# Optimization experiments

Measured on AMD Instinct MI355X. Metric: run time of the kernel, lower is better.

Reference implementation:

```python
import jax, jax.numpy as jnp
import numpy as np

B, S, D = 4, 4096, 1024
P = int(D * 1.333)  # 1364, matches torch int(d_model * proj_factor)
CAP = 15.0
EPS = 1e-6


def _rmsnorm(x, w, eps=EPS):
    xf = x.astype(jnp.float32)
    var = jnp.mean(xf * xf, axis=-1, keepdims=True)
    return w * (xf * jax.lax.rsqrt(var + eps)).astype(x.dtype)


def _softcap_sigmoid(g):
    # sigmoid(cap * tanh(g / cap))
    return jax.nn.sigmoid(CAP * jnp.tanh(g / CAP))


def setup_inputs() -> dict:
    key = jax.random.key(0)
    k0, k1, k2, k3 = jax.random.split(key, 4)
    x = jax.random.normal(k0, (B, S, D), jnp.float32)
    hidden_state = jnp.zeros((B, P), jnp.float32)
    ln_weight = jnp.ones((D,), jnp.float32)
    W_gate = jax.random.normal(k1, (D, 3 * P), jnp.float32) / np.sqrt(D).astype(np.float32)
    W_cell = jax.random.normal(k2, (D, P), jnp.float32) / np.sqrt(D).astype(np.float32)
    W_out = jax.random.normal(k3, (P, D), jnp.float32) / np.sqrt(P).astype(np.float32)
    return {"x": x, "hidden_state": hidden_state, "ln_weight": ln_weight,
            "W_gate": W_gate, "W_cell": W_cell, "W_out": W_out}


def reference(x, hidden_state, ln_weight, W_gate, W_cell, W_out):
    b, s, d = x.shape
    residual = x
    xn = _rmsnorm(x, ln_weight)
    # gate projection -> [b, s, 3, P], unbind gate types
    gates = jnp.einsum('bsd,dk->bsk', xn, W_gate).reshape(b, s, 3, P)
    i_gate = _softcap_sigmoid(gates[:, :, 0])
    f_gate = _softcap_sigmoid(gates[:, :, 1])
    o_gate = _softcap_sigmoid(gates[:, :, 2])
    c_input = jnp.einsum('bsd,dp->bsp', xn, W_cell)

    # sequential linear recurrence: h_t = f_t * h_{t-1} + i_t * tanh(c_t)
    def step(h, inp):
        c_t, i_t, f_t, o_t = inp
        h = f_t * h + i_t * jnp.tanh(c_t)
        return h, o_t * jnp.tanh(h)

    seq = (jnp.swapaxes(c_input, 0, 1), jnp.swapaxes(i_gate, 0, 1),
           jnp.swapaxes(f_gate, 0, 1), jnp.swapaxes(o_gate, 0, 1))  # time-major [s,b,P]
    _, outs = jax.lax.scan(step, hidden_state, seq)
    outputs = jnp.swapaxes(outs, 0, 1)  # [b, s, P]

    out = residual + jnp.einsum('bsp,pd->bsd', outputs, W_out)
    # NOTE: original torch module returns the UNMODIFIED initial hidden_state
    return out, hidden_state
```

## Files before the change

### kernel.cpp

```cpp
#include <hip/hip_runtime.h>
#include <hip/hip_bf16.h>
#include <math.h>
#include <stdint.h>

typedef __bf16 bf16_t;
typedef bf16_t bf16x4 __attribute__((ext_vector_type(4)));
typedef bf16_t bf16x8 __attribute__((ext_vector_type(8)));
typedef float floatx4 __attribute__((ext_vector_type(4)));

#define B_     4
#define S_     4096
#define D_     1024
#define P_     1364
#define P3_    4092
#define NP_    5456
#define NPAD_  5504
#define NB_    5632
#define KPAD_  1408
#define ROWS_  16384
#define CAP_   15.0f
#define EPS_   1e-6f
#define CHUNKS_ 32
#define CLEN_   128

__device__ __forceinline__ float fast_tanh(float x) {
    x = fminf(fmaxf(x, -15.f), 15.f);
    float e = __expf(2.f * x);
    return __fdividef(e - 1.f, e + 1.f);
}
__device__ __forceinline__ float fast_softcap_sig(float g) {
    float t = fast_tanh(g * (1.0f / CAP_));
    return __fdividef(1.f, 1.f + __expf(-CAP_ * t));
}

template <int N>
__device__ __forceinline__ void vmcnt_wait() {
    if constexpr (N == 8)      asm volatile("s_waitcnt vmcnt(8)" ::: "memory");
    else if constexpr (N == 0) asm volatile("s_waitcnt vmcnt(0)" ::: "memory");
}

__global__ __launch_bounds__(256) void rmsnorm_kernel(const float* __restrict__ x,
                                                      const float* __restrict__ w,
                                                      bf16_t* __restrict__ xn) {
    int row = blockIdx.x;
    int tid = threadIdx.x;
    const float4 v = ((const float4*)(x + (size_t)row * D_))[tid];
    float ss = v.x * v.x + v.y * v.y + v.z * v.z + v.w * v.w;
    #pragma unroll
    for (int off = 32; off > 0; off >>= 1) ss += __shfl_down(ss, off);
    __shared__ float red[4];
    if ((tid & 63) == 0) red[tid >> 6] = ss;
    __syncthreads();
    float tot = red[0] + red[1] + red[2] + red[3];
    float scale = rsqrtf(tot * (1.0f / (float)D_) + EPS_);
    const float4 wv = ((const float4*)w)[tid];
    bf16x4 o;
    o[0] = (bf16_t)(v.x * scale * wv.x);
    o[1] = (bf16_t)(v.y * scale * wv.y);
    o[2] = (bf16_t)(v.z * scale * wv.z);
    o[3] = (bf16_t)(v.w * scale * wv.w);
    ((bf16x4*)(xn + (size_t)row * D_))[tid] = o;
}

__global__ __launch_bounds__(256) void pack_wcat(const float* __restrict__ Wg,
                                                 const float* __restrict__ Wc,
                                                 bf16_t* __restrict__ Wt) {
    __shared__ float tile[32][33];
    int kt = blockIdx.x * 32;
    int nt = blockIdx.y * 32;
    int tx = threadIdx.x & 31;
    int ty = threadIdx.x >> 5;
    #pragma unroll
    for (int i = 0; i < 4; i++) {
        int k = kt + ty + 8 * i;
        int n = nt + tx;
        float val = 0.f;
        if (n < P3_)      val = Wg[(size_t)k * P3_ + n];
        else if (n < NP_) val = Wc[(size_t)k * P_ + (n - P3_)];
        tile[ty + 8 * i][tx] = val;
    }
    __syncthreads();
    #pragma unroll
    for (int i = 0; i < 4; i++) {
        int n = nt + ty + 8 * i;
        int k = kt + tx;
        Wt[(size_t)n * D_ + k] = (bf16_t)tile[tx][ty + 8 * i];
    }
}

__global__ __launch_bounds__(256) void pack_wout(const float* __restrict__ Wo,
                                                 bf16_t* __restrict__ Wt) {
    __shared__ float tile[32][33];
    int pt = blockIdx.x * 32;
    int dt = blockIdx.y * 32;
    int tx = threadIdx.x & 31;
    int ty = threadIdx.x >> 5;
    #pragma unroll
    for (int i = 0; i < 4; i++) {
        int p = pt + ty + 8 * i;
        int d = dt + tx;
        float val = (p < P_) ? Wo[(size_t)p * D_ + d] : 0.f;
        tile[ty + 8 * i][tx] = val;
    }
    __syncthreads();
    #pragma unroll
    for (int i = 0; i < 4; i++) {
        int d = dt + ty + 8 * i;
        int p = pt + tx;
        Wt[(size_t)d * KPAD_ + p] = (bf16_t)tile[tx][ty + 8 * i];
    }
}

template <int KTOT, int LDA, int LDB, int LDC, int NX, int EPI>
__global__ __launch_bounds__(512, 2) void gemm8(const bf16_t* __restrict__ A,
                                                const bf16_t* __restrict__ Bt,
                                                const float* __restrict__ res,
                                                void* __restrict__ outv) {
    constexpr int NT = KTOT / 64;
    static_assert(NT >= 4, "NT >= 4");
    __shared__ __align__(16) char smem[131072];

    const int tid  = threadIdx.x;
    const int wid  = tid >> 6;
    const int lane = tid & 63;
    const int l15  = lane & 15;
    const int sl4  = lane >> 4;
    const int sp    = sl4 ^ ((lane >> 1) & 3);
    const int chunk = (lane & 3) ^ ((lane >> 3) & 3);
    const int wrow = (wid >> 2) * 128;
    const int wcol = (wid & 3) * 64;

    constexpr int MCH = (ROWS_ / 256) / 8;
    const int bid = blockIdx.x;
    const int xcd = bid & 7;
    const int idx = bid >> 3;
    const int bx  = idx / MCH;
    const int by  = xcd * MCH + (idx - bx * MCH);
    const int m0 = by * 256, n0 = bx * 256;

    const int srow = wid * 16 + (lane >> 2);
    const bf16_t* Asrc = A  + (size_t)(m0 + srow) * LDA + chunk * 8;
    const bf16_t* Bsrc = Bt + (size_t)(n0 + srow) * LDB + chunk * 8;
    const unsigned ldsA0 = (unsigned)(wid * 1024);
    const unsigned ldsB0 = 32768u + (unsigned)(wid * 1024);

    auto stage = [&](int kt, int buf) {
        #pragma unroll
        for (int kk = 0; kk < 2; kk++) {
            const bf16_t* sa = Asrc + kt * 64 + kk * 32;
            char* da = smem + ((unsigned)buf * 65536u + (unsigned)kk * 16384u + ldsA0);
            __builtin_amdgcn_global_load_lds((const unsigned*)sa, (unsigned*)da, 16, 0, 0);
            __builtin_amdgcn_global_load_lds((const unsigned*)(sa + (size_t)128 * LDA),
                                             (unsigned*)(da + 8192), 16, 0, 0);
            const bf16_t* sb = Bsrc + kt * 64 + kk * 32;
            char* db = smem + ((unsigned)buf * 65536u + (unsigned)kk * 16384u + ldsB0);
            __builtin_amdgcn_global_load_lds((const unsigned*)sb, (unsigned*)db, 16, 0, 0);
            __builtin_amdgcn_global_load_lds((const unsigned*)(sb + (size_t)128 * LDB),
                                             (unsigned*)(db + 8192), 16, 0, 0);
        }
    };
    auto ldA = [&](int buf, int kk, int m) -> bf16x8 {
        return *(const bf16x8*)(smem + (buf * 65536 + kk * 16384 +
                                        (wrow + m * 16 + l15) * 64 + sp * 16));
    };
    auto ldB = [&](int buf, int kk, int n) -> bf16x8 {
        return *(const bf16x8*)(smem + (buf * 65536 + 32768 + kk * 16384 +
                                        (wcol + n * 16 + l15) * 64 + sp * 16));
    };

    floatx4 acc[8][4];
    #pragma unroll
    for (int m = 0; m < 8; m++)
        #pragma unroll
        for (int n = 0; n < 4; n++) acc[m][n] = (floatx4){0.f, 0.f, 0.f, 0.f};

    bf16x8 a0[8], b0v[4], a1[8], b1v[4];

    stage(0, 0);
    stage(1, 1);
    vmcnt_wait<8>();
    __builtin_amdgcn_s_barrier();

    for (int t = 0; t < NT; ++t) {
        const int c = t & 1;
        #pragma unroll
        for (int m = 0; m < 8; m++) a0[m] = ldA(c, 0, m);
        #pragma unroll
        for (int n = 0; n < 4; n++) b0v[n] = ldB(c, 0, n);
        #pragma unroll
        for (int m = 0; m < 8; m++) a1[m] = ldA(c, 1, m);
        #pragma unroll
        for (int n = 0; n < 4; n++) b1v[n] = ldB(c, 1, n);

        __builtin_amdgcn_s_setprio(1);
        #pragma unroll
        for (int m = 0; m < 8; m++)
            #pragma unroll
            for (int n = 0; n < 4; n++)
                acc[m][n] = __builtin_amdgcn_mfma_f32_16x16x32_bf16(a0[m], b0v[n], acc[m][n], 0, 0, 0);
        #pragma unroll
        for (int m = 0; m < 8; m++)
            #pragma unroll
            for (int n = 0; n < 4; n++)
                acc[m][n] = __builtin_amdgcn_mfma_f32_16x16x32_bf16(a1[m], b1v[n], acc[m][n], 0, 0, 0);
        __builtin_amdgcn_s_setprio(0);

        __builtin_amdgcn_s_barrier();
        if (t + 2 < NT) {
            stage(t + 2, c);
            vmcnt_wait<8>();
        } else if (t + 2 == NT) {
            vmcnt_wait<0>();
        }
        __builtin_amdgcn_s_barrier();
    }

    const int crow = m0 + wrow + sl4 * 4;
    const int ccol = n0 + wcol + l15;
    if constexpr (EPI == 0) {
        bf16_t* O = (bf16_t*)outv;
        #pragma unroll
        for (int m = 0; m < 8; m++)
            #pragma unroll
            for (int n = 0; n < 4; n++) {
                const int col = ccol + n * 16;
                if (col < NPAD_) {
                    #pragma unroll
                    for (int r = 0; r < 4; r++) {
                        const int row = crow + m * 16 + r;
                        float g = acc[m][n][r];
                        float v = (col < P3_) ? fast_softcap_sig(g) : fast_tanh(g);
                        O[(size_t)row * LDC + col] = (bf16_t)v;
                    }
                }
            }
    } else {
        float* O = (float*)outv;
        #pragma unroll
        for (int m = 0; m < 8; m++)
            #pragma unroll
            for (int n = 0; n < 4; n++) {
                const int col = ccol + n * 16;
                #pragma unroll
                for (int r = 0; r < 4; r++) {
                    const int row = crow + m * 16 + r;
                    O[(size_t)row * LDC + col] = res[(size_t)row * LDC + col] + acc[m][n][r];
                }
            }
    }
}

__global__ __launch_bounds__(256) void chunk_scan1(const bf16_t* __restrict__ act,
                                                   float* __restrict__ FA) {
    int p = blockIdx.x * 256 + threadIdx.x;
    int c = blockIdx.y;
    int b = blockIdx.z;
    if (p >= P_) return;
    const bf16_t* base = act + (size_t)(b * S_ + c * CLEN_) * NPAD_;
    float F = 1.f, Acc = 0.f;
    for (int t = 0; t < CLEN_; t++) {
        const bf16_t* r = base + (size_t)t * NPAD_;
        float iv = (float)r[p];
        float fv = (float)r[P_ + p];
        float tc = (float)r[P3_ + p];
        Acc = fv * Acc + iv * tc;
        F *= fv;
    }
    size_t idx = (((size_t)b * CHUNKS_ + c) * P_ + p) * 2;
    FA[idx]     = F;
    FA[idx + 1] = Acc;
}

__global__ __launch_bounds__(256) void chunk_scan2(const bf16_t* __restrict__ act,
                                                   const float* __restrict__ FA,
                                                   const float* __restrict__ h0,
                                                   bf16_t* __restrict__ outp) {
    int p = blockIdx.x * 256 + threadIdx.x;
    int c = blockIdx.y;
    int b = blockIdx.z;
    if (p >= KPAD_) return;
    if (p >= P_) {
        bf16_t z = (bf16_t)0.f;
        for (int t = 0; t < CLEN_; t++)
            outp[(size_t)(b * S_ + c * CLEN_ + t) * KPAD_ + p] = z;
        return;
    }
    float h = h0[(size_t)b * P_ + p];
    for (int j = 0; j < c; j++) {
        size_t idx = (((size_t)b * CHUNKS_ + j) * P_ + p) * 2;
        h = FA[idx + 1] + FA[idx] * h;
    }
    const bf16_t* base = act + (size_t)(b * S_ + c * CLEN_) * NPAD_;
    bf16_t* ob = outp + (size_t)(b * S_ + c * CLEN_) * KPAD_;
    for (int t = 0; t < CLEN_; t++) {
        const bf16_t* r = base + (size_t)t * NPAD_;
        float iv = (float)r[p];
        float fv = (float)r[P_ + p];
        float ov = (float)r[2 * P_ + p];
        float tc = (float)r[P3_ + p];
        h = fv * h + iv * tc;
        ob[(size_t)t * KPAD_ + p] = (bf16_t)(ov * fast_tanh(h));
    }
}

__global__ void copy_hidden(const float* __restrict__ hs, float* __restrict__ dst) {
    int i = blockIdx.x * 256 + threadIdx.x;
    if (i < B_ * P_) dst[i] = hs[i];
}

extern "C" void kernel_launch(void* const* d_in, const int* in_sizes, int n_in,
                              void* d_out, int out_size, void* d_ws, size_t ws_size,
                              hipStream_t stream) {
    const float* x   = (const float*)d_in[0];
    const float* hs  = (const float*)d_in[1];
    const float* lnw = (const float*)d_in[2];
    const float* Wg  = (const float*)d_in[3];
    const float* Wc  = (const float*)d_in[4];
    const float* Wo  = (const float*)d_in[5];
    float* out = (float*)d_out;

    char* ws = (char*)d_ws;
    size_t off = 0;
    auto alloc = [&](size_t bytes) {
        void* p = ws + off;
        off += (bytes + 255) & ~(size_t)255;
        return p;
    };
    bf16_t* xn_outp = (bf16_t*)alloc((size_t)ROWS_ * KPAD_ * 2);
    bf16_t* act     = (bf16_t*)alloc((size_t)ROWS_ * NPAD_ * 2);
    bf16_t* WcatT   = (bf16_t*)alloc((size_t)NB_ * D_ * 2);
    bf16_t* WoutT   = (bf16_t*)alloc((size_t)D_ * KPAD_ * 2);
    float*  FA      = (float*)alloc((size_t)B_ * CHUNKS_ * P_ * 2 * 4);

    bf16_t* xn   = xn_outp;
    bf16_t* outp = xn_outp;

    hipLaunchKernelGGL(rmsnorm_kernel, dim3(ROWS_), dim3(256), 0, stream, x, lnw, xn);
    hipLaunchKernelGGL(pack_wcat, dim3(32, NB_ / 32), dim3(256), 0, stream, Wg, Wc, WcatT);
    hipLaunchKernelGGL(pack_wout, dim3(KPAD_ / 32, D_ / 32), dim3(256), 0, stream, Wo, WoutT);

    hipLaunchKernelGGL((gemm8<D_, D_, D_, NPAD_, NB_ / 256, 0>),
                       dim3((NB_ / 256) * (ROWS_ / 256)), dim3(512), 0, stream,
                       xn, WcatT, (const float*)nullptr, (void*)act);

    hipLaunchKernelGGL(chunk_scan1, dim3(6, CHUNKS_, B_), dim3(256), 0, stream, act, FA);
    hipLaunchKernelGGL(chunk_scan2, dim3(6, CHUNKS_, B_), dim3(256), 0, stream, act, FA, hs, outp);

    hipLaunchKernelGGL((gemm8<KPAD_, KPAD_, KPAD_, D_, D_ / 256, 1>),
                       dim3((D_ / 256) * (ROWS_ / 256)), dim3(512), 0, stream,
                       outp, WoutT, x, d_out);

    hipLaunchKernelGGL(copy_hidden, dim3((B_ * P_ + 255) / 256), dim3(256), 0, stream,
                       hs, out + (size_t)ROWS_ * D_);
}
```

Measured before the change: 501.6 us.

## Restructure GEMM main loop into four quadrant phases with interleaved prefetch

Replaces the two-stage-ahead prefetch and monolithic per-tile MFMA block with a one-stage-ahead double buffer. Each k-tile is split into four quadrant sub-phases that interleave LDS fragment reads, A/B global-to-LDS staging and MFMA bursts, with barriers and setprio around each. The aim is to cut register pressure from holding all fragments at once and to spread memory traffic across the compute. In exchange it adds many more barriers per iteration and only one tile of prefetch lead, which may expose global load latency.

```diff
diff --git a/kernel.cpp b/kernel.cpp
--- a/kernel.cpp
+++ b/kernel.cpp
@@ -33,10 +33,8 @@
     return __fdividef(1.f, 1.f + __expf(-CAP_ * t));
 }
 
-template <int N>
-__device__ __forceinline__ void vmcnt_wait() {
-    if constexpr (N == 8)      asm volatile("s_waitcnt vmcnt(8)" ::: "memory");
-    else if constexpr (N == 0) asm volatile("s_waitcnt vmcnt(0)" ::: "memory");
+__device__ __forceinline__ void vmcnt0() {
+    asm volatile("s_waitcnt vmcnt(0)" ::: "memory");
 }
 
 __global__ __launch_bounds__(256) void rmsnorm_kernel(const float* __restrict__ x,
@@ -117,7 +115,7 @@
                                                 const float* __restrict__ res,
                                                 void* __restrict__ outv) {
     constexpr int NT = KTOT / 64;
-    static_assert(NT >= 4, "NT >= 4");
+    static_assert(NT >= 2, "NT >= 2");
     __shared__ __align__(16) char smem[131072];
 
     const int tid  = threadIdx.x;
@@ -144,7 +142,7 @@
     const unsigned ldsA0 = (unsigned)(wid * 1024);
     const unsigned ldsB0 = 32768u + (unsigned)(wid * 1024);
 
-    auto stage = [&](int kt, int buf) {
+    auto stageA = [&](int kt, int buf) {
         #pragma unroll
         for (int kk = 0; kk < 2; kk++) {
             const bf16_t* sa = Asrc + kt * 64 + kk * 32;
@@ -152,6 +150,11 @@
             __builtin_amdgcn_global_load_lds((const unsigned*)sa, (unsigned*)da, 16, 0, 0);
             __builtin_amdgcn_global_load_lds((const unsigned*)(sa + (size_t)128 * LDA),
                                              (unsigned*)(da + 8192), 16, 0, 0);
+        }
+    };
+    auto stageB = [&](int kt, int buf) {
+        #pragma unroll
+        for (int kk = 0; kk < 2; kk++) {
             const bf16_t* sb = Bsrc + kt * 64 + kk * 32;
             char* db = smem + ((unsigned)buf * 65536u + (unsigned)kk * 16384u + ldsB0);
             __builtin_amdgcn_global_load_lds((const unsigned*)sb, (unsigned*)db, 16, 0, 0);
@@ -174,44 +177,82 @@
         #pragma unroll
         for (int n = 0; n < 4; n++) acc[m][n] = (floatx4){0.f, 0.f, 0.f, 0.f};
 
-    bf16x8 a0[8], b0v[4], a1[8], b1v[4];
-
-    stage(0, 0);
-    stage(1, 1);
-    vmcnt_wait<8>();
+    bf16x8 aq[8];
+    bf16x8 bq[4];
+    bf16x8 bq2[4];
+
+    stageA(0, 0);
+    stageB(0, 0);
+    vmcnt0();
     __builtin_amdgcn_s_barrier();
 
     for (int t = 0; t < NT; ++t) {
         const int c = t & 1;
-        #pragma unroll
-        for (int m = 0; m < 8; m++) a0[m] = ldA(c, 0, m);
-        #pragma unroll
-        for (int n = 0; n < 4; n++) b0v[n] = ldB(c, 0, n);
-        #pragma unroll
-        for (int m = 0; m < 8; m++) a1[m] = ldA(c, 1, m);
-        #pragma unroll
-        for (int n = 0; n < 4; n++) b1v[n] = ldB(c, 1, n);
-
+        const bool st = (t + 1 < NT);
+
+        #pragma unroll
+        for (int m = 0; m < 4; m++) { aq[m] = ldA(c, 0, m); aq[m + 4] = ldA(c, 1, m); }
+        #pragma unroll
+        for (int n = 0; n < 2; n++) { bq[n] = ldB(c, 0, n); bq[n + 2] = ldB(c, 1, n); }
+        if (st) stageA(t + 1, c ^ 1);
+        __builtin_amdgcn_s_barrier();
+        asm volatile("s_waitcnt lgkmcnt(0)" ::: "memory");
         __builtin_amdgcn_s_setprio(1);
         #pragma unroll
-        for (int m = 0; m < 8; m++)
-            #pragma unroll
-            for (int n = 0; n < 4; n++)
-                acc[m][n] = __builtin_amdgcn_mfma_f32_16x16x32_bf16(a0[m], b0v[n], acc[m][n], 0, 0, 0);
-        #pragma unroll
-        for (int m = 0; m < 8; m++)
-            #pragma unroll
-            for (int n = 0; n < 4; n++)
-                acc[m][n] = __builtin_amdgcn_mfma_f32_16x16x32_bf16(a1[m], b1v[n], acc[m][n], 0, 0, 0);
+        for (int m = 0; m < 4; m++)
+            #pragma unroll
+            for (int n = 0; n < 2; n++) {
+                acc[m][n] = __builtin_amdgcn_mfma_f32_16x16x32_bf16(aq[m], bq[n], acc[m][n], 0, 0, 0);
+                acc[m][n] = __builtin_amdgcn_mfma_f32_16x16x32_bf16(aq[m + 4], bq[n + 2], acc[m][n], 0, 0, 0);
+            }
         __builtin_amdgcn_s_setprio(0);
-
-        __builtin_amdgcn_s_barrier();
-        if (t + 2 < NT) {
-            stage(t + 2, c);
-            vmcnt_wait<8>();
-        } else if (t + 2 == NT) {
-            vmcnt_wait<0>();
-        }
+        __builtin_amdgcn_s_barrier();
+
+        #pragma unroll
+        for (int n = 0; n < 2; n++) { bq2[n] = ldB(c, 0, n + 2); bq2[n + 2] = ldB(c, 1, n + 2); }
+        if (st) stageB(t + 1, c ^ 1);
+        __builtin_amdgcn_s_barrier();
+        asm volatile("s_waitcnt lgkmcnt(0)" ::: "memory");
+        __builtin_amdgcn_s_setprio(1);
+        #pragma unroll
+        for (int m = 0; m < 4; m++)
+            #pragma unroll
+            for (int n = 0; n < 2; n++) {
+                acc[m][n + 2] = __builtin_amdgcn_mfma_f32_16x16x32_bf16(aq[m], bq2[n], acc[m][n + 2], 0, 0, 0);
+                acc[m][n + 2] = __builtin_amdgcn_mfma_f32_16x16x32_bf16(aq[m + 4], bq2[n + 2], acc[m][n + 2], 0, 0, 0);
+            }
+        __builtin_amdgcn_s_setprio(0);
+        __builtin_amdgcn_s_barrier();
+
+        #pragma unroll
+        for (int m = 0; m < 4; m++) { aq[m] = ldA(c, 0, m + 4); aq[m + 4] = ldA(c, 1, m + 4); }
+        __builtin_amdgcn_s_barrier();
+        asm volatile("s_waitcnt lgkmcnt(0)" ::: "memory");
+        __builtin_amdgcn_s_setprio(1);
+        #pragma unroll
+        for (int m = 0; m < 4; m++)
+            #pragma unroll
+            for (int n = 0; n < 2; n++) {
+                acc[m + 4][n + 2] = __builtin_amdgcn_mfma_f32_16x16x32_bf16(aq[m], bq2[n], acc[m + 4][n + 2], 0, 0, 0);
+                acc[m + 4][n + 2] = __builtin_amdgcn_mfma_f32_16x16x32_bf16(aq[m + 4], bq2[n + 2], acc[m + 4][n + 2], 0, 0, 0);
+            }
+        __builtin_amdgcn_s_setprio(0);
+        __builtin_amdgcn_s_barrier();
+
+        #pragma unroll
+        for (int n = 0; n < 2; n++) { bq[n] = ldB(c, 0, n); bq[n + 2] = ldB(c, 1, n); }
+        __builtin_amdgcn_s_barrier();
+        asm volatile("s_waitcnt lgkmcnt(0)" ::: "memory");
+        __builtin_amdgcn_s_setprio(1);
+        #pragma unroll
+        for (int m = 0; m < 4; m++)
+            #pragma unroll
+            for (int n = 0; n < 2; n++) {
+                acc[m + 4][n] = __builtin_amdgcn_mfma_f32_16x16x32_bf16(aq[m], bq[n], acc[m + 4][n], 0, 0, 0);
+                acc[m + 4][n] = __builtin_amdgcn_mfma_f32_16x16x32_bf16(aq[m + 4], bq[n + 2], acc[m + 4][n], 0, 0, 0);
+            }
+        __builtin_amdgcn_s_setprio(0);
+        vmcnt0();
         __builtin_amdgcn_s_barrier();
     }
 
```

New measurement: 463.5 us. 1.08x faster.

## Replace 256x256 double-buffered GEMM with simpler single-buffered 128x128 tile GEMM

Applied to the files above, without the earlier changes.

Both GEMMs move from a 512-thread kernel with 256x256 output tiles, two LDS stages and hand-placed vmcnt waits to a 256-thread kernel with 128x128 tiles and one LDS stage guarded by __syncthreads. The smaller tile and LDS footprint give more blocks and higher occupancy, and the grid has more blocks to spread across CUs. In exchange it loses load/compute overlap inside a block, halves data reuse per tile (more global and LDS traffic per FLOP), and adds two full barriers per k-step. The result is likely a less efficient GEMM.

```diff
diff --git a/kernel.cpp b/kernel.cpp
--- a/kernel.cpp
+++ b/kernel.cpp
@@ -33,12 +33,6 @@
     return __fdividef(1.f, 1.f + __expf(-CAP_ * t));
 }
 
-template <int N>
-__device__ __forceinline__ void vmcnt_wait() {
-    if constexpr (N == 8)      asm volatile("s_waitcnt vmcnt(8)" ::: "memory");
-    else if constexpr (N == 0) asm volatile("s_waitcnt vmcnt(0)" ::: "memory");
-}
-
 __global__ __launch_bounds__(256) void rmsnorm_kernel(const float* __restrict__ x,
                                                       const float* __restrict__ w,
                                                       bf16_t* __restrict__ xn) {
@@ -111,14 +105,13 @@
     }
 }
 
-template <int KTOT, int LDA, int LDB, int LDC, int NX, int EPI>
-__global__ __launch_bounds__(512, 2) void gemm8(const bf16_t* __restrict__ A,
-                                                const bf16_t* __restrict__ Bt,
-                                                const float* __restrict__ res,
-                                                void* __restrict__ outv) {
+template <int KTOT, int LDA, int LDB, int LDC, int EPI>
+__global__ __launch_bounds__(256) void gemm128(const bf16_t* __restrict__ A,
+                                               const bf16_t* __restrict__ Bt,
+                                               const float* __restrict__ res,
+                                               void* __restrict__ outv) {
     constexpr int NT = KTOT / 64;
-    static_assert(NT >= 4, "NT >= 4");
-    __shared__ __align__(16) char smem[131072];
+    __shared__ __align__(16) char smem[32768];
 
     const int tid  = threadIdx.x;
     const int wid  = tid >> 6;
@@ -127,92 +120,66 @@
     const int sl4  = lane >> 4;
     const int sp    = sl4 ^ ((lane >> 1) & 3);
     const int chunk = (lane & 3) ^ ((lane >> 3) & 3);
-    const int wrow = (wid >> 2) * 128;
-    const int wcol = (wid & 3) * 64;
-
-    constexpr int MCH = (ROWS_ / 256) / 8;
+    const int wrow = (wid >> 1) * 64;
+    const int wcol = (wid & 1) * 64;
+
     const int bid = blockIdx.x;
     const int xcd = bid & 7;
     const int idx = bid >> 3;
-    const int bx  = idx / MCH;
-    const int by  = xcd * MCH + (idx - bx * MCH);
-    const int m0 = by * 256, n0 = bx * 256;
+    const int bx  = idx >> 4;
+    const int by  = xcd * 16 + (idx & 15);
+    const int m0 = by * 128, n0 = bx * 128;
 
     const int srow = wid * 16 + (lane >> 2);
     const bf16_t* Asrc = A  + (size_t)(m0 + srow) * LDA + chunk * 8;
     const bf16_t* Bsrc = Bt + (size_t)(n0 + srow) * LDB + chunk * 8;
-    const unsigned ldsA0 = (unsigned)(wid * 1024);
-    const unsigned ldsB0 = 32768u + (unsigned)(wid * 1024);
-
-    auto stage = [&](int kt, int buf) {
+    const unsigned ldsW = (unsigned)(wid * 1024);
+
+    auto stage = [&](int kt) {
         #pragma unroll
         for (int kk = 0; kk < 2; kk++) {
             const bf16_t* sa = Asrc + kt * 64 + kk * 32;
-            char* da = smem + ((unsigned)buf * 65536u + (unsigned)kk * 16384u + ldsA0);
+            char* da = smem + (unsigned)kk * 8192u + ldsW;
             __builtin_amdgcn_global_load_lds((const unsigned*)sa, (unsigned*)da, 16, 0, 0);
-            __builtin_amdgcn_global_load_lds((const unsigned*)(sa + (size_t)128 * LDA),
-                                             (unsigned*)(da + 8192), 16, 0, 0);
+            __builtin_amdgcn_global_load_lds((const unsigned*)(sa + (size_t)64 * LDA),
+                                             (unsigned*)(da + 4096), 16, 0, 0);
             const bf16_t* sb = Bsrc + kt * 64 + kk * 32;
-            char* db = smem + ((unsigned)buf * 65536u + (unsigned)kk * 16384u + ldsB0);
+            char* db = smem + 16384u + (unsigned)kk * 8192u + ldsW;
             __builtin_amdgcn_global_load_lds((const unsigned*)sb, (unsigned*)db, 16, 0, 0);
-            __builtin_amdgcn_global_load_lds((const unsigned*)(sb + (size_t)128 * LDB),
-                                             (unsigned*)(db + 8192), 16, 0, 0);
+            __builtin_amdgcn_global_load_lds((const unsigned*)(sb + (size_t)64 * LDB),
+                                             (unsigned*)(db + 4096), 16, 0, 0);
         }
     };
-    auto ldA = [&](int buf, int kk, int m) -> bf16x8 {
-        return *(const bf16x8*)(smem + (buf * 65536 + kk * 16384 +
-                                        (wrow + m * 16 + l15) * 64 + sp * 16));
+    auto ldA = [&](int kk, int m) -> bf16x8 {
+        return *(const bf16x8*)(smem + kk * 8192 + (wrow + m * 16 + l15) * 64 + sp * 16);
     };
-    auto ldB = [&](int buf, int kk, int n) -> bf16x8 {
-        return *(const bf16x8*)(smem + (buf * 65536 + 32768 + kk * 16384 +
-                                        (wcol + n * 16 + l15) * 64 + sp * 16));
+    auto ldB = [&](int kk, int n) -> bf16x8 {
+        return *(const bf16x8*)(smem + 16384 + kk * 8192 + (wcol + n * 16 + l15) * 64 + sp * 16);
     };
 
-    floatx4 acc[8][4];
-    #pragma unroll
-    for (int m = 0; m < 8; m++)
+    floatx4 acc[4][4];
+    #pragma unroll
+    for (int m = 0; m < 4; m++)
         #pragma unroll
         for (int n = 0; n < 4; n++) acc[m][n] = (floatx4){0.f, 0.f, 0.f, 0.f};
 
-    bf16x8 a0[8], b0v[4], a1[8], b1v[4];
-
-    stage(0, 0);
-    stage(1, 1);
-    vmcnt_wait<8>();
-    __builtin_amdgcn_s_barrier();
-
     for (int t = 0; t < NT; ++t) {
-        const int c = t & 1;
-        #pragma unroll
-        for (int m = 0; m < 8; m++) a0[m] = ldA(c, 0, m);
-        #pragma unroll
-        for (int n = 0; n < 4; n++) b0v[n] = ldB(c, 0, n);
-        #pragma unroll
-        for (int m = 0; m < 8; m++) a1[m] = ldA(c, 1, m);
-        #pragma unroll
-        for (int n = 0; n < 4; n++) b1v[n] = ldB(c, 1, n);
-
-        __builtin_amdgcn_s_setprio(1);
-        #pragma unroll
-        for (int m = 0; m < 8; m++)
-            #pragma unroll
-            for (int n = 0; n < 4; n++)
-                acc[m][n] = __builtin_amdgcn_mfma_f32_16x16x32_bf16(a0[m], b0v[n], acc[m][n], 0, 0, 0);
-        #pragma unroll
-        for (int m = 0; m < 8; m++)
-            #pragma unroll
-            for (int n = 0; n < 4; n++)
-                acc[m][n] = __builtin_amdgcn_mfma_f32_16x16x32_bf16(a1[m], b1v[n], acc[m][n], 0, 0, 0);
-        __builtin_amdgcn_s_setprio(0);
-
-        __builtin_amdgcn_s_barrier();
-        if (t + 2 < NT) {
-            stage(t + 2, c);
-            vmcnt_wait<8>();
-        } else if (t + 2 == NT) {
-            vmcnt_wait<0>();
+        stage(t);
+        __syncthreads();
+        #pragma unroll
+        for (int kk = 0; kk < 2; kk++) {
+            bf16x8 af[4], bfr[4];
+            #pragma unroll
+            for (int m = 0; m < 4; m++) af[m] = ldA(kk, m);
+            #pragma unroll
+            for (int n = 0; n < 4; n++) bfr[n] = ldB(kk, n);
+            #pragma unroll
+            for (int m = 0; m < 4; m++)
+                #pragma unroll
+                for (int n = 0; n < 4; n++)
+                    acc[m][n] = __builtin_amdgcn_mfma_f32_16x16x32_bf16(af[m], bfr[n], acc[m][n], 0, 0, 0);
         }
-        __builtin_amdgcn_s_barrier();
+        __syncthreads();
     }
 
     const int crow = m0 + wrow + sl4 * 4;
@@ -220,7 +187,7 @@
     if constexpr (EPI == 0) {
         bf16_t* O = (bf16_t*)outv;
         #pragma unroll
-        for (int m = 0; m < 8; m++)
+        for (int m = 0; m < 4; m++)
             #pragma unroll
             for (int n = 0; n < 4; n++) {
                 const int col = ccol + n * 16;
@@ -237,7 +204,7 @@
     } else {
         float* O = (float*)outv;
         #pragma unroll
-        for (int m = 0; m < 8; m++)
+        for (int m = 0; m < 4; m++)
             #pragma unroll
             for (int n = 0; n < 4; n++) {
                 const int col = ccol + n * 16;
@@ -339,15 +306,15 @@
     hipLaunchKernelGGL(pack_wcat, dim3(32, NB_ / 32), dim3(256), 0, stream, Wg, Wc, WcatT);
     hipLaunchKernelGGL(pack_wout, dim3(KPAD_ / 32, D_ / 32), dim3(256), 0, stream, Wo, WoutT);
 
-    hipLaunchKernelGGL((gemm8<D_, D_, D_, NPAD_, NB_ / 256, 0>),
-                       dim3((NB_ / 256) * (ROWS_ / 256)), dim3(512), 0, stream,
+    hipLaunchKernelGGL((gemm128<D_, D_, D_, NPAD_, 0>),
+                       dim3(128 * (NB_ / 128)), dim3(256), 0, stream,
                        xn, WcatT, (const float*)nullptr, (void*)act);
 
     hipLaunchKernelGGL(chunk_scan1, dim3(6, CHUNKS_, B_), dim3(256), 0, stream, act, FA);
     hipLaunchKernelGGL(chunk_scan2, dim3(6, CHUNKS_, B_), dim3(256), 0, stream, act, FA, hs, outp);
 
-    hipLaunchKernelGGL((gemm8<KPAD_, KPAD_, KPAD_, D_, D_ / 256, 1>),
-                       dim3((D_ / 256) * (ROWS_ / 256)), dim3(512), 0, stream,
+    hipLaunchKernelGGL((gemm128<KPAD_, KPAD_, KPAD_, D_, 1>),
+                       dim3(128 * (D_ / 128)), dim3(256), 0, stream,
                        outp, WoutT, x, d_out);
 
     hipLaunchKernelGGL(copy_hidden, dim3((B_ * P_ + 255) / 256), dim3(256), 0, stream,
```

Result: slower. 519.2 us (+3.5%).
